# Kernel tuning notes

Measured on AMD Instinct MI355X. Metric: run time of the kernel, lower is better.

## Reference

```python
import jax, jax.numpy as jnp
import numpy as np

B, T, E, H, G = 8, 1024, 1024, 16, 4
D = E // H
SCALING = D ** -0.5
READER_W = 0.1  # reader_group_weight


def _heads(x):
    # [B, T, E] -> [B, H, T, D]
    return x.reshape(B, T, H, D).transpose(0, 2, 1, 3)


def setup_inputs() -> dict:
    key = jax.random.key(0)
    ks = jax.random.split(key, 16)
    s = 0.02
    return {
        "hidden_states": jax.random.normal(ks[0], (B, T, E), jnp.float32),
        "reader_token": jax.random.randint(ks[1], (B,), 0, G, dtype=jnp.int32),
        # shared (generic) projections, torch Linear convention: y = x @ W.T + b
        "Wq": jax.random.normal(ks[2], (E, E), jnp.float32) * s,
        "bq": jnp.zeros((E,), jnp.float32),
        "Wk": jax.random.normal(ks[3], (E, E), jnp.float32) * s,
        "bk": jnp.zeros((E,), jnp.float32),
        "Wv": jax.random.normal(ks[4], (E, E), jnp.float32) * s,
        "bv": jnp.zeros((E,), jnp.float32),
        "Wo": jax.random.normal(ks[5], (E, E), jnp.float32) * s,
        "bo": jnp.zeros((E,), jnp.float32),
        # stacked per-reader-group expert projections [G, E, E]
        "RWq": jax.random.normal(ks[6], (G, E, E), jnp.float32) * s,
        "Rbq": jnp.zeros((G, E), jnp.float32),
        "RWk": jax.random.normal(ks[7], (G, E, E), jnp.float32) * s,
        "Rbk": jnp.zeros((G, E), jnp.float32),
        "RWv": jax.random.normal(ks[8], (G, E, E), jnp.float32) * s,
        "Rbv": jnp.zeros((G, E), jnp.float32),
    }


def reference(hidden_states, reader_token, Wq, bq, Wk, bk, Wv, bv, Wo, bo,
              RWq, Rbq, RWk, Rbk, RWv, Rbv):
    hs = hidden_states
    # --- generic attention probs (shared weights) ---
    q = _heads((hs @ Wq.T + bq) * SCALING)          # [B,H,T,D]
    k = _heads(hs @ Wk.T + bk)                       # [B,H,T,D]
    v = _heads(hs @ Wv.T + bv)                       # [B,H,T,D]
    gen_probs = jax.nn.softmax(jnp.einsum('bhtd,bhsd->bhts', q, k), axis=-1)
    # --- reader-group attention probs (per-sample routed weights) ---
    Wq_b = RWq[reader_token]                          # [B,E,E]
    Wk_b = RWk[reader_token]
    q_r = _heads((jnp.einsum('bte,boe->bto', hs, Wq_b) + Rbq[reader_token][:, None, :]) * SCALING)
    k_r = _heads(jnp.einsum('bte,boe->bto', hs, Wk_b) + Rbk[reader_token][:, None, :])
    rdr_probs = jax.nn.softmax(jnp.einsum('bhtd,bhsd->bhts', q_r, k_r), axis=-1)
    # --- weighted combine, then attend over GENERIC value states ---
    probs = (READER_W * rdr_probs + (1.0 - READER_W) * gen_probs) / 2.0
    attn = jnp.einsum('bhts,bhsd->bhtd', probs, v)    # [B,H,T,D]
    attn = attn.transpose(0, 2, 1, 3).reshape(B, T, E)
    return attn @ Wo.T + bo
```

## Files before the change

kernel.cpp:

```cpp
#include <hip/hip_runtime.h>
#include <stdint.h>

#define AS1 __attribute__((address_space(1)))
#define AS3 __attribute__((address_space(3)))

typedef __attribute__((ext_vector_type(8))) short bf16x8;
typedef __attribute__((ext_vector_type(4))) float f32x4;

#define NB 8
#define NT 1024
#define NE 1024
#define NH 16
#define BT (NB * NT)

__device__ __forceinline__ unsigned short f2bf(float f) {
    unsigned int u = __builtin_bit_cast(unsigned int, f);
    u += 0x7FFFu + ((u >> 16) & 1u);
    return (unsigned short)(u >> 16);
}
__device__ __forceinline__ unsigned int cvt_pk_bf16(float lo, float hi) {
    unsigned int r;
    asm("v_cvt_pk_bf16_f32 %0, %1, %2" : "=v"(r) : "v"(lo), "v"(hi));
    return r;
}

__global__ void k_cvt7(const float* __restrict__ hs, unsigned short* __restrict__ hsB,
                       const float* __restrict__ w1, unsigned short* __restrict__ w1B,
                       const float* __restrict__ w2, unsigned short* __restrict__ w2B,
                       const float* __restrict__ w3, unsigned short* __restrict__ w3B,
                       const float* __restrict__ w4, unsigned short* __restrict__ w4B,
                       const float* __restrict__ r1, unsigned short* __restrict__ r1B,
                       const float* __restrict__ r2, unsigned short* __restrict__ r2B)
{
    int blk = blockIdx.x;
    const float* s; unsigned short* d; int base;
    if      (blk < 8192)  { s = hs; d = hsB; base = 0; }
    else if (blk < 9216)  { s = w1; d = w1B; base = 8192; }
    else if (blk < 10240) { s = w2; d = w2B; base = 9216; }
    else if (blk < 11264) { s = w3; d = w3B; base = 10240; }
    else if (blk < 12288) { s = w4; d = w4B; base = 11264; }
    else if (blk < 16384) { s = r1; d = r1B; base = 12288; }
    else                  { s = r2; d = r2B; base = 16384; }
    int i = ((blk - base) * 256 + threadIdx.x) * 4;
    float4 f = *reinterpret_cast<const float4*>(s + i);
    ushort4 o;
    o.x = f2bf(f.x); o.y = f2bf(f.y); o.z = f2bf(f.z); o.w = f2bf(f.w);
    *reinterpret_cast<ushort4*>(d + i) = o;
}

struct GJob {
    const unsigned short* W;
    const float* bias;
    void* out;
    float scale;
    int routed;
};

template <bool OUT_F32>
__global__ __launch_bounds__(512, 2)
void k_gemm256(const unsigned short* __restrict__ A,
               GJob j0, GJob j1, GJob j2, GJob j3, GJob j4,
               const int* __restrict__ rt)
{
    __shared__ __attribute__((aligned(16))) unsigned short LB[2][2][2][128 * 64];

    const int flat = blockIdx.x;
    const int xcd = flat & 7;
    const int l   = flat >> 3;
    const int pz  = l >> 4;
    const int r   = l & 15;
    const int by  = xcd * 4 + (r >> 2);
    const int bx  = r & 3;
    const int m0 = by << 8, n0 = bx << 8;

    GJob jb = j0;
    if (pz == 1) jb = j1;
    else if (pz == 2) jb = j2;
    else if (pz == 3) jb = j3;
    else if (pz == 4) jb = j4;
    int g = jb.routed ? rt[m0 >> 10] : 0;
    const unsigned short* Wg = jb.W + (size_t)g * NE * NE;

    const int tid  = threadIdx.x;
    const int wid  = tid >> 6;
    const int lane = tid & 63;
    const int frow = lane & 15;
    const int g4   = lane >> 4;
    const int wm = wid >> 2, wn = wid & 3;

    const int rh0  = tid >> 3;
    const int swz8 = ((tid & 7) ^ (rh0 & 7)) * 8;
    const unsigned short* baseA = A  + (size_t)m0 * NE;
    const unsigned short* baseB = Wg + (size_t)n0 * NE;

    auto STAGE = [&](int d, int mat, int half, int kt) {
        const unsigned short* base = mat ? baseB : baseA;
#pragma unroll
        for (int j = 0; j < 2; ++j) {
            const unsigned short* src =
                base + (size_t)(half * 128 + rh0 + j * 64) * NE + kt * 64 + swz8;
            __builtin_amdgcn_global_load_lds((AS1 void*)src,
                (AS3 void*)&LB[d][mat][half][(wid * 64 + j * 512) * 8], 16, 0, 0);
        }
    };

    f32x4 acc[8][4];
#pragma unroll
    for (int m = 0; m < 8; ++m)
#pragma unroll
        for (int n = 0; n < 4; ++n) acc[m][n] = (f32x4){0.f, 0.f, 0.f, 0.f};

    bf16x8 a4[4], b4[4];
    auto RDA = [&](int d, int mh, int kh) {
#pragma unroll
        for (int mf = 0; mf < 4; ++mf) {
            int rh = mh * 64 + mf * 16 + frow;
            int off = rh * 64 + (((kh * 4 + g4) ^ (frow & 7)) * 8);
            a4[mf] = *reinterpret_cast<const bf16x8*>(&LB[d][0][wm][off]);
        }
    };
    auto RDB = [&](int d, int kh) {
#pragma unroll
        for (int nf = 0; nf < 4; ++nf) {
            int rh = (wn & 1) * 64 + nf * 16 + frow;
            int off = rh * 64 + (((kh * 4 + g4) ^ (frow & 7)) * 8);
            b4[nf] = *reinterpret_cast<const bf16x8*>(&LB[d][1][wn >> 1][off]);
        }
    };
    auto MM = [&](int mh) {
        __builtin_amdgcn_s_setprio(1);
#pragma unroll
        for (int mf = 0; mf < 4; ++mf)
#pragma unroll
            for (int nf = 0; nf < 4; ++nf)
                acc[mh * 4 + mf][nf] =
                    __builtin_amdgcn_mfma_f32_16x16x32_bf16(a4[mf], b4[nf], acc[mh * 4 + mf][nf], 0, 0, 0);
        __builtin_amdgcn_s_setprio(0);
    };

#define BARX __builtin_amdgcn_s_barrier()
#define LGK0 asm volatile("s_waitcnt lgkmcnt(0)" ::: "memory")
#define VMC2 asm volatile("s_waitcnt vmcnt(2)" ::: "memory")

    STAGE(0, 0, 0, 0); STAGE(0, 0, 1, 0); STAGE(0, 1, 0, 0); STAGE(0, 1, 1, 0);
    STAGE(1, 1, 0, 1);
    VMC2; BARX;

#pragma unroll 1
    for (int i = 0; i < 8; ++i) {
        const int t = 2 * i;
        const bool pre = (i < 7);
        RDA(0, 0, 0); RDB(0, 0); STAGE(1, 1, 1, t + 1);
        BARX; LGK0; MM(0); BARX;
        RDA(0, 1, 0); STAGE(1, 0, 0, t + 1);
        BARX; LGK0; MM(1); BARX;
        RDA(0, 0, 1); RDB(0, 1); STAGE(1, 0, 1, t + 1);
        BARX; LGK0; MM(0); BARX;
        RDA(0, 1, 1); if (pre) STAGE(0, 1, 0, t + 2);
        BARX; LGK0; MM(1); VMC2; BARX;
        RDA(1, 0, 0); RDB(1, 0); if (pre) STAGE(0, 1, 1, t + 2);
        BARX; LGK0; MM(0); BARX;
        RDA(1, 1, 0); if (pre) STAGE(0, 0, 0, t + 2);
        BARX; LGK0; MM(1); BARX;
        RDA(1, 0, 1); RDB(1, 1); if (pre) STAGE(0, 0, 1, t + 2);
        BARX; LGK0; MM(0); BARX;
        RDA(1, 1, 1); if (pre) STAGE(1, 1, 0, t + 3);
        BARX; LGK0; MM(1); VMC2; BARX;
    }
#undef BARX
#undef LGK0
#undef VMC2

    const float* biasg = jb.bias + (size_t)(jb.routed ? (rt[m0 >> 10]) : 0) * NE;
#pragma unroll
    for (int am = 0; am < 8; ++am) {
        int row = m0 + wm * 128 + am * 16 + g4 * 4;
#pragma unroll
        for (int nf = 0; nf < 4; ++nf) {
            int col = n0 + wn * 64 + nf * 16 + frow;
            float bv = biasg[col];
            f32x4 v = acc[am][nf];
#pragma unroll
            for (int r2 = 0; r2 < 4; ++r2) {
                float val = (v[r2] + bv) * jb.scale;
                if (OUT_F32)
                    ((float*)jb.out)[(size_t)(row + r2) * NE + col] = val;
                else
                    ((unsigned short*)jb.out)[(size_t)(row + r2) * NE + col] = f2bf(val);
            }
        }
    }
}

__global__ void k_vtrans(const unsigned short* __restrict__ V, unsigned short* __restrict__ Vt) {
    __shared__ unsigned short tile[64][65];
    const int blk = blockIdx.x;
    const int bh = blk >> 4;
    const int b = bh >> 4;
    const int h = bh & 15;
    const int s0 = (blk & 15) * 64;
    const int tid = threadIdx.x;
#pragma unroll
    for (int i = 0; i < 2; ++i) {
        int seg = tid + i * 256;
        int row = seg >> 3;
        int c8 = (seg & 7) * 8;
        const unsigned short* src = V + (size_t)(b * NT + s0 + row) * NE + h * 64 + c8;
        ushort4 u0 = *reinterpret_cast<const ushort4*>(src);
        ushort4 u1 = *reinterpret_cast<const ushort4*>(src + 4);
        tile[row][c8 + 0] = u0.x; tile[row][c8 + 1] = u0.y;
        tile[row][c8 + 2] = u0.z; tile[row][c8 + 3] = u0.w;
        tile[row][c8 + 4] = u1.x; tile[row][c8 + 5] = u1.y;
        tile[row][c8 + 6] = u1.z; tile[row][c8 + 7] = u1.w;
    }
    __syncthreads();
#pragma unroll
    for (int i = 0; i < 2; ++i) {
        int seg = tid + i * 256;
        int drow = seg >> 3;
        int s8 = (seg & 7) * 8;
        ushort4 u0, u1;
        u0.x = tile[s8 + 0][drow]; u0.y = tile[s8 + 1][drow];
        u0.z = tile[s8 + 2][drow]; u0.w = tile[s8 + 3][drow];
        u1.x = tile[s8 + 4][drow]; u1.y = tile[s8 + 5][drow];
        u1.z = tile[s8 + 6][drow]; u1.w = tile[s8 + 7][drow];
        unsigned short* dst = Vt + (size_t)(bh * 64 + drow) * NT + s0 + s8;
        *reinterpret_cast<ushort4*>(dst) = u0;
        *reinterpret_cast<ushort4*>(dst + 4) = u1;
    }
}

__global__ __launch_bounds__(512, 4)
void k_attn(const unsigned short* __restrict__ Q,
            const unsigned short* __restrict__ K,
            const unsigned short* __restrict__ Qr,
            const unsigned short* __restrict__ Kr,
            const unsigned short* __restrict__ Vt,
            unsigned short* __restrict__ attnO)
{
    constexpr int PLD = 40;
    __shared__ __attribute__((aligned(16))) unsigned short KV[2][3 * 4096];
    __shared__ __attribute__((aligned(16))) unsigned short Pga[8][16 * PLD];
    __shared__ __attribute__((aligned(16))) unsigned short Pra[8][16 * PLD];

    const int blk = (blockIdx.x & 7) * 128 + (blockIdx.x >> 3);
    const int tile = blk & 7;
    const int bh = blk >> 3;
    const int b = bh >> 4;
    const int h = bh & 15;
    const int wid = threadIdx.x >> 6;
    const int lane = threadIdx.x & 63;
    const int frow = lane & 15;
    const int g4 = lane >> 4;
    const int f7 = frow & 7;
    const int fk8 = g4 * 8;
    const int t0 = tile * 128 + wid * 16;

    const size_t qoff = (size_t)(b * NT + t0 + frow) * NE + h * 64;
    const bf16x8 qf0 = *reinterpret_cast<const bf16x8*>(Q + qoff + fk8);
    const bf16x8 qf1 = *reinterpret_cast<const bf16x8*>(Q + qoff + 32 + fk8);
    const bf16x8 qr0 = *reinterpret_cast<const bf16x8*>(Qr + qoff + fk8);
    const bf16x8 qr1 = *reinterpret_cast<const bf16x8*>(Qr + qoff + 32 + fk8);

    const unsigned short* Kb  = K  + (size_t)b * NT * NE + h * 64;
    const unsigned short* Krb = Kr + (size_t)b * NT * NE + h * 64;
    const unsigned short* Vtb = Vt + (size_t)bh * 64 * NT;
    unsigned short* PgRow = &Pga[wid][0] + frow * PLD;
    unsigned short* PrRow = &Pra[wid][0] + frow * PLD;

    f32x4 og[4], orr[4];
    float lgp = 0.f, lrp = 0.f;
#pragma unroll
    for (int i = 0; i < 4; ++i) {
        og[i] = (f32x4){0.f, 0.f, 0.f, 0.f};
        orr[i] = (f32x4){0.f, 0.f, 0.f, 0.f};
    }

    const int srow = threadIdx.x >> 3;
    const int scb8 = ((threadIdx.x & 7) ^ (srow & 7)) * 8;
    auto stage = [&](int buf, int s0) {
        const unsigned short* sK = Kb  + (size_t)(s0 + srow) * NE + scb8;
        const unsigned short* sR = Krb + (size_t)(s0 + srow) * NE + scb8;
        const unsigned short* sV = Vtb + (size_t)srow * NT + s0 + scb8;
        __builtin_amdgcn_global_load_lds((AS1 void*)sK, (AS3 void*)(&KV[buf][wid * 512]), 16, 0, 0);
        __builtin_amdgcn_global_load_lds((AS1 void*)sR, (AS3 void*)(&KV[buf][4096 + wid * 512]), 16, 0, 0);
        __builtin_amdgcn_global_load_lds((AS1 void*)sV, (AS3 void*)(&KV[buf][8192 + wid * 512]), 16, 0, 0);
    };

    stage(0, 0);
    __syncthreads();
    int cur = 0;
    const f32x4 z = (f32x4){0.f, 0.f, 0.f, 0.f};
#pragma unroll 1
    for (int t = 0; t < NT / 64; ++t) {
        if (t < NT / 64 - 1) stage(cur ^ 1, (t + 1) * 64);
        const unsigned short* Kl  = &KV[cur][0];
        const unsigned short* Krl = &KV[cur][4096];
        const unsigned short* Vl  = &KV[cur][8192];

        f32x4 sg[4], sr[4];
#pragma unroll
        for (int nf = 0; nf < 4; ++nf) {
            const int ro = (nf * 16 + frow) * 64;
            bf16x8 kA = *reinterpret_cast<const bf16x8*>(Kl + ro + ((g4 ^ f7) * 8));
            bf16x8 kB = *reinterpret_cast<const bf16x8*>(Kl + ro + (((4 + g4) ^ f7) * 8));
            bf16x8 rA = *reinterpret_cast<const bf16x8*>(Krl + ro + ((g4 ^ f7) * 8));
            bf16x8 rB = *reinterpret_cast<const bf16x8*>(Krl + ro + (((4 + g4) ^ f7) * 8));
            sg[nf] = __builtin_amdgcn_mfma_f32_16x16x32_bf16(kA, qf0, z, 0, 0, 0);
            sg[nf] = __builtin_amdgcn_mfma_f32_16x16x32_bf16(kB, qf1, sg[nf], 0, 0, 0);
            sr[nf] = __builtin_amdgcn_mfma_f32_16x16x32_bf16(rA, qr0, z, 0, 0, 0);
            sr[nf] = __builtin_amdgcn_mfma_f32_16x16x32_bf16(rB, qr1, sr[nf], 0, 0, 0);
        }

#pragma unroll
        for (int hh = 0; hh < 2; ++hh) {
#pragma unroll
            for (int j = 0; j < 2; ++j) {
                const int nf = 2 * hh + j;
                float g0 = __expf(sg[nf][0]), g1 = __expf(sg[nf][1]);
                float g2 = __expf(sg[nf][2]), g3 = __expf(sg[nf][3]);
                lgp += (g0 + g1) + (g2 + g3);
                uint2 wg;
                wg.x = cvt_pk_bf16(g0, g1);
                wg.y = cvt_pk_bf16(g2, g3);
                *reinterpret_cast<uint2*>(PgRow + j * 16 + g4 * 4) = wg;
                float r0 = __expf(sr[nf][0]), r1 = __expf(sr[nf][1]);
                float r2 = __expf(sr[nf][2]), r3 = __expf(sr[nf][3]);
                lrp += (r0 + r1) + (r2 + r3);
                uint2 wr;
                wr.x = cvt_pk_bf16(r0, r1);
                wr.y = cvt_pk_bf16(r2, r3);
                *reinterpret_cast<uint2*>(PrRow + j * 16 + g4 * 4) = wr;
            }
            asm volatile("s_waitcnt lgkmcnt(0)" ::: "memory");
            bf16x8 pg = *reinterpret_cast<const bf16x8*>(PgRow + fk8);
            bf16x8 pr = *reinterpret_cast<const bf16x8*>(PrRow + fk8);
            __builtin_amdgcn_s_setprio(1);
#pragma unroll
            for (int nf2 = 0; nf2 < 4; ++nf2) {
                const int vo = (nf2 * 16 + frow) * 64;
                bf16x8 v = *reinterpret_cast<const bf16x8*>(Vl + vo + (((4 * hh + g4) ^ f7) * 8));
                og[nf2]  = __builtin_amdgcn_mfma_f32_16x16x32_bf16(pg, v, og[nf2], 0, 0, 0);
                orr[nf2] = __builtin_amdgcn_mfma_f32_16x16x32_bf16(pr, v, orr[nf2], 0, 0, 0);
            }
            __builtin_amdgcn_s_setprio(0);
        }

        __syncthreads();
        cur ^= 1;
    }

    lgp += __shfl_xor(lgp, 16); lgp += __shfl_xor(lgp, 32);
    lrp += __shfl_xor(lrp, 16); lrp += __shfl_xor(lrp, 32);
    float ig = 0.45f / lgp, ir = 0.05f / lrp;
    float igr[4], irr[4];
#pragma unroll
    for (int r = 0; r < 4; ++r) {
        igr[r] = __shfl(ig, g4 * 4 + r);
        irr[r] = __shfl(ir, g4 * 4 + r);
    }
#pragma unroll
    for (int nf2 = 0; nf2 < 4; ++nf2) {
#pragma unroll
        for (int r = 0; r < 4; ++r) {
            float val = og[nf2][r] * igr[r] + orr[nf2][r] * irr[r];
            int tq = t0 + g4 * 4 + r;
            attnO[(size_t)(b * NT + tq) * NE + h * 64 + nf2 * 16 + frow] = f2bf(val);
        }
    }
}

extern "C" void kernel_launch(void* const* d_in, const int* in_sizes, int n_in,
                              void* d_out, int out_size, void* d_ws, size_t ws_size,
                              hipStream_t stream)
{
    const float* hs  = (const float*)d_in[0];
    const int*   rt  = (const int*)d_in[1];
    const float* Wq  = (const float*)d_in[2];
    const float* bq  = (const float*)d_in[3];
    const float* Wk  = (const float*)d_in[4];
    const float* bk  = (const float*)d_in[5];
    const float* Wv  = (const float*)d_in[6];
    const float* bv  = (const float*)d_in[7];
    const float* Wo  = (const float*)d_in[8];
    const float* bo  = (const float*)d_in[9];
    const float* RWq = (const float*)d_in[10];
    const float* Rbq = (const float*)d_in[11];
    const float* RWk = (const float*)d_in[12];
    const float* Rbk = (const float*)d_in[13];

    unsigned short* w = (unsigned short*)d_ws;
    const size_t NBT = (size_t)BT * NE;
    const size_t NW  = (size_t)NE * NE;
    unsigned short* hsB  = w; w += NBT;
    unsigned short* Qb   = w; w += NBT;
    unsigned short* Kb   = w; w += NBT;
    unsigned short* Vb   = w; w += NBT;
    unsigned short* Qrb  = w; w += NBT;
    unsigned short* Krb  = w; w += NBT;
    unsigned short* Vtb  = w; w += NBT;
    unsigned short* atb  = w; w += NBT;
    unsigned short* WqB  = w; w += NW;
    unsigned short* WkB  = w; w += NW;
    unsigned short* WvB  = w; w += NW;
    unsigned short* WoB  = w; w += NW;
    unsigned short* RWqB = w; w += 4 * NW;
    unsigned short* RWkB = w; w += 4 * NW;

    k_cvt7<<<dim3(20480), dim3(256), 0, stream>>>(hs, hsB, Wq, WqB, Wk, WkB, Wv, WvB,
                                                  Wo, WoB, RWq, RWqB, RWk, RWkB);

    GJob jq  = { WqB,  bq,  Qb,  0.125f, 0 };
    GJob jk  = { WkB,  bk,  Kb,  1.0f,   0 };
    GJob jv  = { WvB,  bv,  Vb,  1.0f,   0 };
    GJob jrq = { RWqB, Rbq, Qrb, 0.125f, 1 };
    GJob jrk = { RWkB, Rbk, Krb, 1.0f,   1 };
    k_gemm256<false><<<dim3(640), dim3(512), 0, stream>>>(hsB, jq, jk, jv, jrq, jrk, rt);

    k_vtrans<<<dim3(NB * NH * 16), dim3(256), 0, stream>>>(Vb, Vtb);
    k_attn<<<dim3(NB * NH * 8), dim3(512), 0, stream>>>(Qb, Kb, Qrb, Krb, Vtb, atb);

    GJob jo = { WoB, bo, d_out, 1.0f, 0 };
    k_gemm256<true><<<dim3(128), dim3(512), 0, stream>>>(atb, jo, jo, jo, jo, jo, nullptr);
}
```

Measured before the change: 240.2 us.

## Process 32 query rows per wave in attention to reuse K/V fragments

The attention kernel now runs 4 waves (256 threads) per block, and each wave handles 32 query rows instead of 16. Each K, Kr and V fragment read from LDS therefore feeds twice as many MFMAs. The two separate P scratch buffers are merged into one per-wave buffer that is reused in turn for the generic and reader probabilities. Staging is split into two loads per thread. The cost is more accumulator registers per wave and fewer waves to hide latency, and the serialized reuse of the P buffer adds an extra wait.

New measurement: 242.7 us. No clear change (+1.1%).

```diff
diff --git a/kernel.cpp b/kernel.cpp
--- a/kernel.cpp
+++ b/kernel.cpp
@@ -230,7 +230,7 @@
     }
 }
 
-__global__ __launch_bounds__(512, 4)
+__global__ __launch_bounds__(256, 2)
 void k_attn(const unsigned short* __restrict__ Q,
             const unsigned short* __restrict__ K,
             const unsigned short* __restrict__ Qr,
@@ -240,51 +240,61 @@
 {
     constexpr int PLD = 40;
     __shared__ __attribute__((aligned(16))) unsigned short KV[2][3 * 4096];
-    __shared__ __attribute__((aligned(16))) unsigned short Pga[8][16 * PLD];
-    __shared__ __attribute__((aligned(16))) unsigned short Pra[8][16 * PLD];
+    __shared__ __attribute__((aligned(16))) unsigned short Ps[4][32 * PLD];
 
     const int blk = (blockIdx.x & 7) * 128 + (blockIdx.x >> 3);
     const int tile = blk & 7;
     const int bh = blk >> 3;
     const int b = bh >> 4;
     const int h = bh & 15;
-    const int wid = threadIdx.x >> 6;
-    const int lane = threadIdx.x & 63;
+    const int tid = threadIdx.x;
+    const int wid = tid >> 6;
+    const int lane = tid & 63;
     const int frow = lane & 15;
     const int g4 = lane >> 4;
     const int f7 = frow & 7;
     const int fk8 = g4 * 8;
-    const int t0 = tile * 128 + wid * 16;
-
-    const size_t qoff = (size_t)(b * NT + t0 + frow) * NE + h * 64;
-    const bf16x8 qf0 = *reinterpret_cast<const bf16x8*>(Q + qoff + fk8);
-    const bf16x8 qf1 = *reinterpret_cast<const bf16x8*>(Q + qoff + 32 + fk8);
-    const bf16x8 qr0 = *reinterpret_cast<const bf16x8*>(Qr + qoff + fk8);
-    const bf16x8 qr1 = *reinterpret_cast<const bf16x8*>(Qr + qoff + 32 + fk8);
+    const int t0 = tile * 128 + wid * 32;
+
+    bf16x8 qf[2][2], qr[2][2];
+#pragma unroll
+    for (int qh = 0; qh < 2; ++qh) {
+        const size_t qoff = (size_t)(b * NT + t0 + qh * 16 + frow) * NE + h * 64;
+        qf[qh][0] = *reinterpret_cast<const bf16x8*>(Q + qoff + fk8);
+        qf[qh][1] = *reinterpret_cast<const bf16x8*>(Q + qoff + 32 + fk8);
+        qr[qh][0] = *reinterpret_cast<const bf16x8*>(Qr + qoff + fk8);
+        qr[qh][1] = *reinterpret_cast<const bf16x8*>(Qr + qoff + 32 + fk8);
+    }
 
     const unsigned short* Kb  = K  + (size_t)b * NT * NE + h * 64;
     const unsigned short* Krb = Kr + (size_t)b * NT * NE + h * 64;
     const unsigned short* Vtb = Vt + (size_t)bh * 64 * NT;
-    unsigned short* PgRow = &Pga[wid][0] + frow * PLD;
-    unsigned short* PrRow = &Pra[wid][0] + frow * PLD;
-
-    f32x4 og[4], orr[4];
-    float lgp = 0.f, lrp = 0.f;
-#pragma unroll
-    for (int i = 0; i < 4; ++i) {
-        og[i] = (f32x4){0.f, 0.f, 0.f, 0.f};
-        orr[i] = (f32x4){0.f, 0.f, 0.f, 0.f};
-    }
-
-    const int srow = threadIdx.x >> 3;
-    const int scb8 = ((threadIdx.x & 7) ^ (srow & 7)) * 8;
+    unsigned short* Pw = &Ps[wid][0];
+
+    f32x4 og[2][4], orr[2][4];
+    float lgp[2] = {0.f, 0.f}, lrp[2] = {0.f, 0.f};
+#pragma unroll
+    for (int qh = 0; qh < 2; ++qh)
+#pragma unroll
+        for (int i = 0; i < 4; ++i) {
+            og[qh][i] = (f32x4){0.f, 0.f, 0.f, 0.f};
+            orr[qh][i] = (f32x4){0.f, 0.f, 0.f, 0.f};
+        }
+
     auto stage = [&](int buf, int s0) {
-        const unsigned short* sK = Kb  + (size_t)(s0 + srow) * NE + scb8;
-        const unsigned short* sR = Krb + (size_t)(s0 + srow) * NE + scb8;
-        const unsigned short* sV = Vtb + (size_t)srow * NT + s0 + scb8;
-        __builtin_amdgcn_global_load_lds((AS1 void*)sK, (AS3 void*)(&KV[buf][wid * 512]), 16, 0, 0);
-        __builtin_amdgcn_global_load_lds((AS1 void*)sR, (AS3 void*)(&KV[buf][4096 + wid * 512]), 16, 0, 0);
-        __builtin_amdgcn_global_load_lds((AS1 void*)sV, (AS3 void*)(&KV[buf][8192 + wid * 512]), 16, 0, 0);
+#pragma unroll
+        for (int j = 0; j < 2; ++j) {
+            int c = tid + j * 256;
+            int row = c >> 3, cb = c & 7;
+            int off = (cb ^ (row & 7)) * 8;
+            const unsigned short* sK = Kb  + (size_t)(s0 + row) * NE + off;
+            const unsigned short* sR = Krb + (size_t)(s0 + row) * NE + off;
+            const unsigned short* sV = Vtb + (size_t)row * NT + s0 + off;
+            const int dst = (wid * 64 + j * 256) * 8;
+            __builtin_amdgcn_global_load_lds((AS1 void*)sK, (AS3 void*)(&KV[buf][dst]), 16, 0, 0);
+            __builtin_amdgcn_global_load_lds((AS1 void*)sR, (AS3 void*)(&KV[buf][4096 + dst]), 16, 0, 0);
+            __builtin_amdgcn_global_load_lds((AS1 void*)sV, (AS3 void*)(&KV[buf][8192 + dst]), 16, 0, 0);
+        }
     };
 
     stage(0, 0);
@@ -298,7 +308,7 @@
         const unsigned short* Krl = &KV[cur][4096];
         const unsigned short* Vl  = &KV[cur][8192];
 
-        f32x4 sg[4], sr[4];
+        f32x4 sg[2][4], sr[2][4];
 #pragma unroll
         for (int nf = 0; nf < 4; ++nf) {
             const int ro = (nf * 16 + frow) * 64;
@@ -306,66 +316,102 @@
             bf16x8 kB = *reinterpret_cast<const bf16x8*>(Kl + ro + (((4 + g4) ^ f7) * 8));
             bf16x8 rA = *reinterpret_cast<const bf16x8*>(Krl + ro + ((g4 ^ f7) * 8));
             bf16x8 rB = *reinterpret_cast<const bf16x8*>(Krl + ro + (((4 + g4) ^ f7) * 8));
-            sg[nf] = __builtin_amdgcn_mfma_f32_16x16x32_bf16(kA, qf0, z, 0, 0, 0);
-            sg[nf] = __builtin_amdgcn_mfma_f32_16x16x32_bf16(kB, qf1, sg[nf], 0, 0, 0);
-            sr[nf] = __builtin_amdgcn_mfma_f32_16x16x32_bf16(rA, qr0, z, 0, 0, 0);
-            sr[nf] = __builtin_amdgcn_mfma_f32_16x16x32_bf16(rB, qr1, sr[nf], 0, 0, 0);
+#pragma unroll
+            for (int qh = 0; qh < 2; ++qh) {
+                sg[qh][nf] = __builtin_amdgcn_mfma_f32_16x16x32_bf16(kA, qf[qh][0], z, 0, 0, 0);
+                sg[qh][nf] = __builtin_amdgcn_mfma_f32_16x16x32_bf16(kB, qf[qh][1], sg[qh][nf], 0, 0, 0);
+                sr[qh][nf] = __builtin_amdgcn_mfma_f32_16x16x32_bf16(rA, qr[qh][0], z, 0, 0, 0);
+                sr[qh][nf] = __builtin_amdgcn_mfma_f32_16x16x32_bf16(rB, qr[qh][1], sr[qh][nf], 0, 0, 0);
+            }
         }
 
 #pragma unroll
         for (int hh = 0; hh < 2; ++hh) {
-#pragma unroll
-            for (int j = 0; j < 2; ++j) {
-                const int nf = 2 * hh + j;
-                float g0 = __expf(sg[nf][0]), g1 = __expf(sg[nf][1]);
-                float g2 = __expf(sg[nf][2]), g3 = __expf(sg[nf][3]);
-                lgp += (g0 + g1) + (g2 + g3);
-                uint2 wg;
-                wg.x = cvt_pk_bf16(g0, g1);
-                wg.y = cvt_pk_bf16(g2, g3);
-                *reinterpret_cast<uint2*>(PgRow + j * 16 + g4 * 4) = wg;
-                float r0 = __expf(sr[nf][0]), r1 = __expf(sr[nf][1]);
-                float r2 = __expf(sr[nf][2]), r3 = __expf(sr[nf][3]);
-                lrp += (r0 + r1) + (r2 + r3);
-                uint2 wr;
-                wr.x = cvt_pk_bf16(r0, r1);
-                wr.y = cvt_pk_bf16(r2, r3);
-                *reinterpret_cast<uint2*>(PrRow + j * 16 + g4 * 4) = wr;
+            bf16x8 v4[4];
+#pragma unroll
+            for (int nf2 = 0; nf2 < 4; ++nf2)
+                v4[nf2] = *reinterpret_cast<const bf16x8*>(
+                    Vl + (nf2 * 16 + frow) * 64 + (((4 * hh + g4) ^ f7) * 8));
+
+#pragma unroll
+            for (int qh = 0; qh < 2; ++qh) {
+                unsigned short* Prow = Pw + (qh * 16 + frow) * PLD;
+#pragma unroll
+                for (int j = 0; j < 2; ++j) {
+                    const int nf = 2 * hh + j;
+                    float p0 = __expf(sg[qh][nf][0]), p1 = __expf(sg[qh][nf][1]);
+                    float p2 = __expf(sg[qh][nf][2]), p3 = __expf(sg[qh][nf][3]);
+                    lgp[qh] += (p0 + p1) + (p2 + p3);
+                    uint2 wv;
+                    wv.x = cvt_pk_bf16(p0, p1);
+                    wv.y = cvt_pk_bf16(p2, p3);
+                    *reinterpret_cast<uint2*>(Prow + j * 16 + g4 * 4) = wv;
+                }
             }
             asm volatile("s_waitcnt lgkmcnt(0)" ::: "memory");
-            bf16x8 pg = *reinterpret_cast<const bf16x8*>(PgRow + fk8);
-            bf16x8 pr = *reinterpret_cast<const bf16x8*>(PrRow + fk8);
-            __builtin_amdgcn_s_setprio(1);
-#pragma unroll
-            for (int nf2 = 0; nf2 < 4; ++nf2) {
-                const int vo = (nf2 * 16 + frow) * 64;
-                bf16x8 v = *reinterpret_cast<const bf16x8*>(Vl + vo + (((4 * hh + g4) ^ f7) * 8));
-                og[nf2]  = __builtin_amdgcn_mfma_f32_16x16x32_bf16(pg, v, og[nf2], 0, 0, 0);
-                orr[nf2] = __builtin_amdgcn_mfma_f32_16x16x32_bf16(pr, v, orr[nf2], 0, 0, 0);
-            }
-            __builtin_amdgcn_s_setprio(0);
+            {
+                bf16x8 pg0 = *reinterpret_cast<const bf16x8*>(Pw + frow * PLD + fk8);
+                bf16x8 pg1 = *reinterpret_cast<const bf16x8*>(Pw + (16 + frow) * PLD + fk8);
+                __builtin_amdgcn_s_setprio(1);
+#pragma unroll
+                for (int nf2 = 0; nf2 < 4; ++nf2) {
+                    og[0][nf2] = __builtin_amdgcn_mfma_f32_16x16x32_bf16(pg0, v4[nf2], og[0][nf2], 0, 0, 0);
+                    og[1][nf2] = __builtin_amdgcn_mfma_f32_16x16x32_bf16(pg1, v4[nf2], og[1][nf2], 0, 0, 0);
+                }
+                __builtin_amdgcn_s_setprio(0);
+            }
+#pragma unroll
+            for (int qh = 0; qh < 2; ++qh) {
+                unsigned short* Prow = Pw + (qh * 16 + frow) * PLD;
+#pragma unroll
+                for (int j = 0; j < 2; ++j) {
+                    const int nf = 2 * hh + j;
+                    float p0 = __expf(sr[qh][nf][0]), p1 = __expf(sr[qh][nf][1]);
+                    float p2 = __expf(sr[qh][nf][2]), p3 = __expf(sr[qh][nf][3]);
+                    lrp[qh] += (p0 + p1) + (p2 + p3);
+                    uint2 wv;
+                    wv.x = cvt_pk_bf16(p0, p1);
+                    wv.y = cvt_pk_bf16(p2, p3);
+                    *reinterpret_cast<uint2*>(Prow + j * 16 + g4 * 4) = wv;
+                }
+            }
+            asm volatile("s_waitcnt lgkmcnt(0)" ::: "memory");
+            {
+                bf16x8 pr0 = *reinterpret_cast<const bf16x8*>(Pw + frow * PLD + fk8);
+                bf16x8 pr1 = *reinterpret_cast<const bf16x8*>(Pw + (16 + frow) * PLD + fk8);
+                __builtin_amdgcn_s_setprio(1);
+#pragma unroll
+                for (int nf2 = 0; nf2 < 4; ++nf2) {
+                    orr[0][nf2] = __builtin_amdgcn_mfma_f32_16x16x32_bf16(pr0, v4[nf2], orr[0][nf2], 0, 0, 0);
+                    orr[1][nf2] = __builtin_amdgcn_mfma_f32_16x16x32_bf16(pr1, v4[nf2], orr[1][nf2], 0, 0, 0);
+                }
+                __builtin_amdgcn_s_setprio(0);
+            }
         }
 
         __syncthreads();
         cur ^= 1;
     }
 
-    lgp += __shfl_xor(lgp, 16); lgp += __shfl_xor(lgp, 32);
-    lrp += __shfl_xor(lrp, 16); lrp += __shfl_xor(lrp, 32);
-    float ig = 0.45f / lgp, ir = 0.05f / lrp;
-    float igr[4], irr[4];
-#pragma unroll
-    for (int r = 0; r < 4; ++r) {
-        igr[r] = __shfl(ig, g4 * 4 + r);
-        irr[r] = __shfl(ir, g4 * 4 + r);
-    }
-#pragma unroll
-    for (int nf2 = 0; nf2 < 4; ++nf2) {
+#pragma unroll
+    for (int qh = 0; qh < 2; ++qh) {
+        lgp[qh] += __shfl_xor(lgp[qh], 16); lgp[qh] += __shfl_xor(lgp[qh], 32);
+        lrp[qh] += __shfl_xor(lrp[qh], 16); lrp[qh] += __shfl_xor(lrp[qh], 32);
+        float ig = 0.45f / lgp[qh], ir = 0.05f / lrp[qh];
+        float igr[4], irr[4];
 #pragma unroll
         for (int r = 0; r < 4; ++r) {
-            float val = og[nf2][r] * igr[r] + orr[nf2][r] * irr[r];
-            int tq = t0 + g4 * 4 + r;
-            attnO[(size_t)(b * NT + tq) * NE + h * 64 + nf2 * 16 + frow] = f2bf(val);
+            igr[r] = __shfl(ig, g4 * 4 + r);
+            irr[r] = __shfl(ir, g4 * 4 + r);
+        }
+#pragma unroll
+        for (int nf2 = 0; nf2 < 4; ++nf2) {
+#pragma unroll
+            for (int r = 0; r < 4; ++r) {
+                float val = og[qh][nf2][r] * igr[r] + orr[qh][nf2][r] * irr[r];
+                int tq = t0 + qh * 16 + g4 * 4 + r;
+                attnO[(size_t)(b * NT + tq) * NE + h * 64 + nf2 * 16 + frow] = f2bf(val);
+            }
         }
     }
 }
@@ -418,7 +464,7 @@
     k_gemm256<false><<<dim3(640), dim3(512), 0, stream>>>(hsB, jq, jk, jv, jrq, jrk, rt);
 
     k_vtrans<<<dim3(NB * NH * 16), dim3(256), 0, stream>>>(Vb, Vtb);
-    k_attn<<<dim3(NB * NH * 8), dim3(512), 0, stream>>>(Qb, Kb, Qrb, Krb, Vtb, atb);
+    k_attn<<<dim3(NB * NH * 8), dim3(256), 0, stream>>>(Qb, Kb, Qrb, Krb, Vtb, atb);
 
     GJob jo = { WoB, bo, d_out, 1.0f, 0 };
     k_gemm256<true><<<dim3(128), dim3(512), 0, stream>>>(atb, jo, jo, jo, jo, jo, nullptr);
```
